# Performance work log

Hardware: AMD Instinct MI355X
Metric: run time of the kernel (lower is better)

The kernel has to match this reference:

```python
import jax, jax.numpy as jnp
import numpy as np

N = 150000   # total supergraph nodes (entities+events+chains)
D = 128      # embed_size
H = 4        # attention heads
DH = D // H  # head dim
E = 300000   # edges per layer
L = 4        # layer_specs length
A = 8        # edge attr dim
T = 10       # num_edge_type
TIME_SCALE = 24.0
SLOPE = 0.2  # negative_slope


def setup_inputs() -> dict:
    key = jax.random.key(0)
    ks = jax.random.split(key, 16)
    nrm = lambda k, s, sc=1.0: jax.random.normal(k, s, dtype=jnp.float32) * sc
    return {
        'x': nrm(ks[0], (N, D), 0.1),
        'Wq': nrm(ks[1], (L, D, D), D ** -0.5),
        'Wk': nrm(ks[2], (L, D, D), D ** -0.5),
        'Wv': nrm(ks[3], (L, D, D), D ** -0.5),
        'Wskip': nrm(ks[4], (L, D, D), D ** -0.5),
        'Wa': nrm(ks[5], (L, A, D), 0.1),
        'time_w': nrm(ks[6], (D,)),
        'time_b': nrm(ks[7], (D,), 0.1),
        'dist_w': nrm(ks[8], (D,)),
        'dist_b': nrm(ks[9], (D,), 0.1),
        'type_table': nrm(ks[10], (T, D), 0.1),
        'bn_gamma': jnp.ones((L, D), jnp.float32),
        'bn_beta': jnp.zeros((L, D), jnp.float32),
        'beta': jnp.full((L,), 0.5, jnp.float32),
        'edge_attr': jax.random.uniform(ks[11], (L, E, A), dtype=jnp.float32),
        'edge_dt': jax.random.uniform(ks[12], (L, E), dtype=jnp.float32) * TIME_SCALE,
        'edge_ds': jax.random.uniform(ks[13], (L, E), dtype=jnp.float32) * 10.0,
        'edge_index': jax.random.randint(ks[14], (L, 2, E), 0, N),
        'edge_type': jax.random.randint(ks[15], (L, E), 0, T),
    }


def _layer(x, Wq, Wk, Wv, Wskip, Wa, time_w, time_b, dist_w, dist_b,
           type_table, gamma, bvec, beta, attr, dt, ds, ei, et):
    n = x.shape[0]
    src, dst = ei[0], ei[1]
    # continuous time / distance encoders: cos basis (TimeEncoder / 'time' DistanceEncoder)
    te = jnp.cos((dt / TIME_SCALE)[:, None] * time_w + time_b)   # [E,D]
    de = jnp.cos(ds[:, None] * dist_w + dist_b)                  # [E,D]
    # 'add' edge/time fusion: attr MLP + time + dist + edge-type embeddings
    edge_feat = attr @ Wa + te + de + type_table[et]             # [E,D]
    kv_in = x[src] + edge_feat                                   # gather + fuse
    q = (x @ Wq).reshape(n, H, DH)[dst]                          # [E,H,DH]
    k = (kv_in @ Wk).reshape(-1, H, DH)
    v = (kv_in @ Wv).reshape(-1, H, DH)
    logits = (q * k).sum(-1) * (DH ** -0.5)                      # [E,H]
    logits = jnp.where(logits >= 0, logits, SLOPE * logits)      # leaky_relu(negative_slope)
    # segment softmax over incoming edges of each destination node
    m = jax.ops.segment_max(logits, dst, num_segments=n)
    a = jnp.exp(logits - m[dst])
    denom = jax.ops.segment_sum(a, dst, num_segments=n)
    a = a / denom[dst]
    agg = jax.ops.segment_sum(a[..., None] * v, dst, num_segments=n).reshape(n, D)
    # beta-weighted residual (learn_beta) with skip projection
    out = beta * (x @ Wskip) + (1.0 - beta) * agg
    # BatchNorm1d (training-mode batch stats) + ReLU
    mu = out.mean(0)
    var = out.var(0)
    out = (out - mu) * jax.lax.rsqrt(var + 1e-5) * gamma + bvec
    return jax.nn.relu(out)


def reference(x, Wq, Wk, Wv, Wskip, Wa, time_w, time_b, dist_w, dist_b,
              type_table, bn_gamma, bn_beta, beta, edge_attr, edge_dt,
              edge_ds, edge_index, edge_type):
    for l in range(L):  # entity2event, event2event, event2chain (time filter), chain2chain
        x = _layer(x, Wq[l], Wk[l], Wv[l], Wskip[l], Wa[l],
                   time_w, time_b, dist_w, dist_b, type_table,
                   bn_gamma[l], bn_beta[l], beta[l],
                   edge_attr[l], edge_dt[l], edge_ds[l],
                   edge_index[l], edge_type[l])
    return x
```

## Files before the change

kernel.cpp:

```cpp
#include <hip/hip_runtime.h>

typedef unsigned int u32;
typedef unsigned short u16;
typedef short bf16x8 __attribute__((ext_vector_type(8)));
typedef float f32x4 __attribute__((ext_vector_type(4)));

#define N_NODES 150000
#define E_EDGES 300000
#define L_CNT   151552
#define ETILES  9375
#define NTILES  4688

__device__ __forceinline__ float blo(u32 u){ return __uint_as_float(u << 16); }
__device__ __forceinline__ float bhi(u32 u){ return __uint_as_float(u & 0xffff0000u); }
__device__ __forceinline__ float b2f(u16 h){ return __uint_as_float(((u32)h) << 16); }
__device__ __forceinline__ u16 f2bf(float f){
  u32 u = __float_as_uint(f);
  return (u16)((u + 0x7fffu + ((u >> 16) & 1u)) >> 16);
}
__device__ __forceinline__ u32 pack2(float a, float b){
  return (u32)f2bf(a) | ((u32)f2bf(b) << 16);
}

__device__ __forceinline__ f32x4 mfma16(bf16x8 a, bf16x8 b, f32x4 c){
  return __builtin_amdgcn_mfma_f32_16x16x32_bf16(a, b, c, 0, 0, 0);
}

__device__ __forceinline__ int opsw(int r, int k){ return (r * 128 + k) ^ ((r & 7) << 3); }
__device__ __forceinline__ int csw(int r, int n){ return (r * 128 + n) ^ (((r >> 2) & 3) << 3); }

__global__ __launch_bounds__(256)
void k_wt(const float* __restrict__ Wq, const float* __restrict__ Wk,
          const float* __restrict__ Wv, const float* __restrict__ Ws,
          u16* __restrict__ Wt)
{
  const int m = blockIdx.x;
  const float* src = (m < 4 ? Wq : m < 8 ? Wk : m < 12 ? Wv : Ws)
                     + (size_t)(m & 3) * 16384;
  u16* dst = Wt + (size_t)m * 16384;
  const int t = threadIdx.x;
  for (int i = 0; i < 16; ++i) {
    int idx = i * 256 + t;
    int n = idx >> 5;
    int k4 = (idx & 31) << 2;
    ushort4 o;
    o.x = f2bf(src[(k4 + 0) * 128 + n]);
    o.y = f2bf(src[(k4 + 1) * 128 + n]);
    o.z = f2bf(src[(k4 + 2) * 128 + n]);
    o.w = f2bf(src[(k4 + 3) * 128 + n]);
    *(ushort4*)(dst + n * 128 + k4) = o;
  }
}


__global__ __launch_bounds__(256)
void k_hist(const int* __restrict__ eidx, int* __restrict__ counts)
{
  const int l = blockIdx.y;
  const int e = blockIdx.x * 256 + threadIdx.x;
  if (e < E_EDGES) {
    int dst = eidx[(size_t)l * 2 * E_EDGES + E_EDGES + e];
    atomicAdd(&counts[(size_t)l * L_CNT + dst], 1);
  }
}

__global__ __launch_bounds__(256)
void k_scan1(const int* __restrict__ counts, int* __restrict__ rowptr,
             int* __restrict__ bsum)
{
  __shared__ int sh[256];
  const int b = blockIdx.x, l = blockIdx.y;
  const int t = threadIdx.x;
  const int* c = counts + (size_t)l * L_CNT + b * 2048;
  int* rp = rowptr + (size_t)l * L_CNT + b * 2048;
  int v[8]; int s = 0;
  #pragma unroll
  for (int j = 0; j < 8; ++j) { v[j] = c[t * 8 + j]; s += v[j]; }
  sh[t] = s; __syncthreads();
  for (int off = 1; off < 256; off <<= 1) {
    int x = (t >= off) ? sh[t - off] : 0;
    __syncthreads();
    sh[t] += x;
    __syncthreads();
  }
  int excl = (t == 0) ? 0 : sh[t - 1];
  if (t == 255) bsum[l * 128 + b] = sh[255];
  int run = excl;
  #pragma unroll
  for (int j = 0; j < 8; ++j) { rp[t * 8 + j] = run; run += v[j]; }
}

__global__ __launch_bounds__(128)
void k_scan2(int* __restrict__ bsum)
{
  __shared__ int sh[128];
  const int l = blockIdx.x, t = threadIdx.x;
  int v = (t < 74) ? bsum[l * 128 + t] : 0;
  sh[t] = v; __syncthreads();
  for (int off = 1; off < 128; off <<= 1) {
    int x = (t >= off) ? sh[t - off] : 0;
    __syncthreads();
    sh[t] += x;
    __syncthreads();
  }
  int excl = (t == 0) ? 0 : sh[t - 1];
  if (t < 74) bsum[l * 128 + t] = excl;
}

__global__ __launch_bounds__(256)
void k_scan3(int* __restrict__ rowptr, int* __restrict__ tmp,
             const int* __restrict__ bsum)
{
  const int l = blockIdx.y;
  const int q = blockIdx.x * 256 + threadIdx.x;
  int v = rowptr[(size_t)l * L_CNT + q] + bsum[l * 128 + (q >> 11)];
  rowptr[(size_t)l * L_CNT + q] = v;
  tmp[(size_t)l * L_CNT + q] = v;
}

__global__ __launch_bounds__(256)
void k_scatter(const int* __restrict__ srcP, const int* __restrict__ dstP,
               const int* __restrict__ etP, const float* __restrict__ dtP,
               const float* __restrict__ dsP, const float* __restrict__ attrP,
               int* __restrict__ tmpL, u32* __restrict__ meta)
{
  const int e = blockIdx.x * 256 + threadIdx.x;
  if (e < E_EDGES) {
    int dst = dstP[e];
    int pos = atomicAdd(&tmpL[dst], 1);
    int src = srcP[e];
    int et  = etP[e];
    float dtn = dtP[e] * (1.0f / 24.0f);
    float dsv = dsP[e];
    float4 aA = *(const float4*)(attrP + (size_t)e * 8);
    float4 aB = *(const float4*)(attrP + (size_t)e * 8 + 4);
    uint4 r0, r1;
    r0.x = (u32)src;
    r0.y = (u32)dst | ((u32)et << 20);
    r0.z = __float_as_uint(dtn);
    r0.w = __float_as_uint(dsv);
    r1.x = pack2(aA.x, aA.y); r1.y = pack2(aA.z, aA.w);
    r1.z = pack2(aB.x, aB.y); r1.w = pack2(aB.z, aB.w);
    u32* mp = meta + (size_t)pos * 8;
    *(uint4*)mp = r0;
    *(uint4*)(mp + 4) = r1;
  }
}

template<int XF32>
__global__ __launch_bounds__(256)
void k_kvin(const void* __restrict__ xg, const float* __restrict__ Wa,
            const float* __restrict__ tw, const float* __restrict__ tb,
            const float* __restrict__ dw, const float* __restrict__ db,
            const float* __restrict__ ttab, const u32* __restrict__ meta,
            u16* __restrict__ kvV)
{
  const int idx = blockIdx.x * 256 + threadIdx.x;
  const int e = idx >> 4;
  const int c8 = (idx & 15) << 3;
  const u32* mp = meta + (size_t)e * 8;
  uint4 m0 = *(const uint4*)mp;
  uint4 m1 = *(const uint4*)(mp + 4);
  const int src = (int)m0.x;
  const int et = (int)(m0.y >> 20);
  const float dtn = __uint_as_float(m0.z);
  const float dss = __uint_as_float(m0.w);
  float aa[8] = { blo(m1.x), bhi(m1.x), blo(m1.y), bhi(m1.y),
                  blo(m1.z), bhi(m1.z), blo(m1.w), bhi(m1.w) };
  const float4 twA = *(const float4*)(tw + c8);
  const float4 twB = *(const float4*)(tw + c8 + 4);
  const float4 tbA = *(const float4*)(tb + c8);
  const float4 tbB = *(const float4*)(tb + c8 + 4);
  const float4 dwA = *(const float4*)(dw + c8);
  const float4 dwB = *(const float4*)(dw + c8 + 4);
  const float4 dbA = *(const float4*)(db + c8);
  const float4 dbB = *(const float4*)(db + c8 + 4);
  const float4 ttA = *(const float4*)(ttab + et * 128 + c8);
  const float4 ttB = *(const float4*)(ttab + et * 128 + c8 + 4);
  float f[8];
  f[0] = __cosf(fmaf(dtn, twA.x, tbA.x)) + __cosf(fmaf(dss, dwA.x, dbA.x)) + ttA.x;
  f[1] = __cosf(fmaf(dtn, twA.y, tbA.y)) + __cosf(fmaf(dss, dwA.y, dbA.y)) + ttA.y;
  f[2] = __cosf(fmaf(dtn, twA.z, tbA.z)) + __cosf(fmaf(dss, dwA.z, dbA.z)) + ttA.z;
  f[3] = __cosf(fmaf(dtn, twA.w, tbA.w)) + __cosf(fmaf(dss, dwA.w, dbA.w)) + ttA.w;
  f[4] = __cosf(fmaf(dtn, twB.x, tbB.x)) + __cosf(fmaf(dss, dwB.x, dbB.x)) + ttB.x;
  f[5] = __cosf(fmaf(dtn, twB.y, tbB.y)) + __cosf(fmaf(dss, dwB.y, dbB.y)) + ttB.y;
  f[6] = __cosf(fmaf(dtn, twB.z, tbB.z)) + __cosf(fmaf(dss, dwB.z, dbB.z)) + ttB.z;
  f[7] = __cosf(fmaf(dtn, twB.w, tbB.w)) + __cosf(fmaf(dss, dwB.w, dbB.w)) + ttB.w;
  #pragma unroll
  for (int a = 0; a < 8; ++a) {
    float4 wA = *(const float4*)(Wa + a * 128 + c8);
    float4 wB = *(const float4*)(Wa + a * 128 + c8 + 4);
    f[0] = fmaf(aa[a], wA.x, f[0]);
    f[1] = fmaf(aa[a], wA.y, f[1]);
    f[2] = fmaf(aa[a], wA.z, f[2]);
    f[3] = fmaf(aa[a], wA.w, f[3]);
    f[4] = fmaf(aa[a], wB.x, f[4]);
    f[5] = fmaf(aa[a], wB.y, f[5]);
    f[6] = fmaf(aa[a], wB.z, f[6]);
    f[7] = fmaf(aa[a], wB.w, f[7]);
  }
  float xv[8];
  if (XF32) {
    float4 xA = *(const float4*)((const float*)xg + (size_t)src * 128 + c8);
    float4 xB = *(const float4*)((const float*)xg + (size_t)src * 128 + c8 + 4);
    xv[0] = xA.x; xv[1] = xA.y; xv[2] = xA.z; xv[3] = xA.w;
    xv[4] = xB.x; xv[5] = xB.y; xv[6] = xB.z; xv[7] = xB.w;
  } else {
    uint4 xr = *(const uint4*)((const u16*)xg + (size_t)src * 128 + c8);
    xv[0] = blo(xr.x); xv[1] = bhi(xr.x); xv[2] = blo(xr.y); xv[3] = bhi(xr.y);
    xv[4] = blo(xr.z); xv[5] = bhi(xr.z); xv[6] = blo(xr.w); xv[7] = bhi(xr.w);
  }
  uint4 o;
  o.x = pack2(xv[0] + f[0], xv[1] + f[1]);
  o.y = pack2(xv[2] + f[2], xv[3] + f[3]);
  o.z = pack2(xv[4] + f[4], xv[5] + f[5]);
  o.w = pack2(xv[6] + f[6], xv[7] + f[7]);
  *(uint4*)(kvV + (size_t)e * 128 + c8) = o;
}


template<int XF32>
__global__ __launch_bounds__(128, 2)
void gemm_qs(const void* __restrict__ xg, const u16* __restrict__ WtQ,
             const u16* __restrict__ WtS, u16* __restrict__ Qo,
             u16* __restrict__ So)
{
  __shared__ __align__(16) u16 As[4160];
  __shared__ __align__(16) u16 Bs[4160];
  const int t = threadIdx.x;
  const int w = t >> 6, lane = t & 63;
  const int lr = lane & 15, hi = lane >> 4;
  const int row0 = blockIdx.x * 32;
  const int nr = min(32, N_NODES - row0);
  const u16* Wt = w ? WtS : WtQ;
  u16* C = w ? So : Qo;

  bf16x8 wt[8][4];
  #pragma unroll
  for (int nb = 0; nb < 8; ++nb)
    #pragma unroll
    for (int ks = 0; ks < 4; ++ks)
      wt[nb][ks] = *(const bf16x8*)(Wt + (nb * 16 + lr) * 128 + ks * 32 + hi * 8);

  #pragma unroll
  for (int i = 0; i < 4; ++i) {
    int idx = i * 128 + t;
    int r = idx >> 4, c8 = (idx & 15) << 3;
    if (r < nr) {
      if (XF32) {
        float4 vA = *(const float4*)((const float*)xg + (size_t)(row0 + r) * 128 + c8);
        float4 vB = *(const float4*)((const float*)xg + (size_t)(row0 + r) * 128 + c8 + 4);
        uint4 o;
        o.x = pack2(vA.x, vA.y); o.y = pack2(vA.z, vA.w);
        o.z = pack2(vB.x, vB.y); o.w = pack2(vB.z, vB.w);
        *(uint4*)(As + opsw(r, c8)) = o;
      } else {
        uint4 v = *(const uint4*)((const u16*)xg + (size_t)(row0 + r) * 128 + c8);
        *(uint4*)(As + opsw(r, c8)) = v;
      }
    } else {
      *(uint4*)(As + opsw(r, c8)) = make_uint4(0, 0, 0, 0);
    }
  }
  __syncthreads();

  f32x4 acc[2][8];
  #pragma unroll
  for (int a = 0; a < 2; ++a)
    #pragma unroll
    for (int b = 0; b < 8; ++b) {
      acc[a][b][0] = 0.f; acc[a][b][1] = 0.f;
      acc[a][b][2] = 0.f; acc[a][b][3] = 0.f;
    }
  #pragma unroll
  for (int ks = 0; ks < 4; ++ks) {
    const int kb = ks * 32 + hi * 8;
    bf16x8 a0 = *(const bf16x8*)(As + opsw(lr, kb));
    bf16x8 a1 = *(const bf16x8*)(As + opsw(16 + lr, kb));
    #pragma unroll
    for (int nb = 0; nb < 8; ++nb) {
      acc[0][nb] = mfma16(a0, wt[nb][ks], acc[0][nb]);
      acc[1][nb] = mfma16(a1, wt[nb][ks], acc[1][nb]);
    }
  }
  __syncthreads();

  u16* Cs = w ? Bs : As;
  const int g4 = hi << 2;
  #pragma unroll
  for (int mt = 0; mt < 2; ++mt)
    #pragma unroll
    for (int nt = 0; nt < 8; ++nt)
      #pragma unroll
      for (int j = 0; j < 4; ++j)
        Cs[csw(mt * 16 + g4 + j, nt * 16 + lr)] = f2bf(acc[mt][nt][j]);
  #pragma unroll
  for (int i = 0; i < 8; ++i) {
    int idx = i * 64 + lane;
    int r = idx >> 4, n8 = (idx & 15) << 3;
    if (r < nr) {
      uint4 v = *(const uint4*)(Cs + csw(r, n8));
      *(uint4*)(C + (size_t)(row0 + r) * 128 + n8) = v;
    }
  }
}


__global__ __launch_bounds__(128, 2)
void edge_kv(const u16* __restrict__ WtK, const u16* __restrict__ WtV,
             const u32* __restrict__ meta, const u16* __restrict__ Qb,
             u16* __restrict__ kvV, float* __restrict__ logits)
{
  __shared__ __align__(16) u16 KVs[4160];
  __shared__ __align__(16) u16 Qs[4160];
  __shared__ __align__(16) u16 Cs[4160];
  __shared__ int dstSh[32];
  const int t = threadIdx.x;
  const int w = t >> 6, lane = t & 63;
  const int lr = lane & 15, hi = lane >> 4;
  const int e0 = blockIdx.x * 32;
  const u16* Wt = w ? WtV : WtK;

  bf16x8 wt[8][4];
  #pragma unroll
  for (int nb = 0; nb < 8; ++nb)
    #pragma unroll
    for (int ks = 0; ks < 4; ++ks)
      wt[nb][ks] = *(const bf16x8*)(Wt + (nb * 16 + lr) * 128 + ks * 32 + hi * 8);

  if (t < 32)
    dstSh[t] = (int)(meta[(size_t)(e0 + t) * 8 + 1] & 0xFFFFFu);

  #pragma unroll
  for (int i = 0; i < 4; ++i) {
    int idx = i * 128 + t;
    int r = idx >> 4, c8 = (idx & 15) << 3;
    uint4 v = *(const uint4*)(kvV + (size_t)(e0 + r) * 128 + c8);
    *(uint4*)(KVs + opsw(r, c8)) = v;
  }
  if (w == 0) {
    #pragma unroll
    for (int i = 0; i < 8; ++i) {
      int idx = i * 64 + lane;
      int r = idx >> 4, c8 = (idx & 15) << 3;
      int qrow = dstSh[r];
      uint4 qv = *(const uint4*)(Qb + (size_t)qrow * 128 + c8);
      *(uint4*)(Qs + opsw(r, c8)) = qv;
    }
  }
  __syncthreads();

  if (w == 0) {
    #pragma unroll
    for (int eb = 0; eb < 2; ++eb) {
      f32x4 kacc[8];
      #pragma unroll
      for (int b = 0; b < 8; ++b) {
        kacc[b][0] = 0.f; kacc[b][1] = 0.f; kacc[b][2] = 0.f; kacc[b][3] = 0.f;
      }
      #pragma unroll
      for (int ks = 0; ks < 4; ++ks) {
        bf16x8 ef = *(const bf16x8*)(KVs + opsw(eb * 16 + lr, ks * 32 + hi * 8));
        #pragma unroll
        for (int nb = 0; nb < 8; ++nb)
          kacc[nb] = mfma16(wt[nb][ks], ef, kacc[nb]);
      }
      const int el = eb * 16 + lr;
      float hs[4] = {0.f, 0.f, 0.f, 0.f};
      #pragma unroll
      for (int nb = 0; nb < 8; ++nb) {
        ushort4 q = *(const ushort4*)(Qs + opsw(el, nb * 16 + hi * 4));
        hs[nb >> 1] += b2f(q.x) * kacc[nb][0] + b2f(q.y) * kacc[nb][1]
                     + b2f(q.z) * kacc[nb][2] + b2f(q.w) * kacc[nb][3];
      }
      #pragma unroll
      for (int h = 0; h < 4; ++h) {
        hs[h] += __shfl_xor(hs[h], 16, 64);
        hs[h] += __shfl_xor(hs[h], 32, 64);
        hs[h] *= 0.17677669529663687f;
        hs[h] = (hs[h] >= 0.f) ? hs[h] : 0.2f * hs[h];
      }
      if (lane < 16)
        *(float4*)(logits + (size_t)(e0 + el) * 4) = make_float4(hs[0], hs[1], hs[2], hs[3]);
    }
  } else {
    const int g4 = hi << 2;
    #pragma unroll
    for (int mt = 0; mt < 2; ++mt) {
      f32x4 vacc[8];
      #pragma unroll
      for (int b = 0; b < 8; ++b) {
        vacc[b][0] = 0.f; vacc[b][1] = 0.f; vacc[b][2] = 0.f; vacc[b][3] = 0.f;
      }
      #pragma unroll
      for (int ks = 0; ks < 4; ++ks) {
        bf16x8 af = *(const bf16x8*)(KVs + opsw(mt * 16 + lr, ks * 32 + hi * 8));
        #pragma unroll
        for (int nb = 0; nb < 8; ++nb)
          vacc[nb] = mfma16(af, wt[nb][ks], vacc[nb]);
      }
      #pragma unroll
      for (int nt = 0; nt < 8; ++nt)
        #pragma unroll
        for (int j = 0; j < 4; ++j)
          Cs[csw(mt * 16 + g4 + j, nt * 16 + lr)] = f2bf(vacc[nt][j]);
    }
    #pragma unroll
    for (int i = 0; i < 8; ++i) {
      int idx = i * 64 + lane;
      int r = idx >> 4, n8 = (idx & 15) << 3;
      uint4 v = *(const uint4*)(Cs + csw(r, n8));
      *(uint4*)(kvV + (size_t)(e0 + r) * 128 + n8) = v;
    }
  }
}

__global__ __launch_bounds__(256)
void node_agg(const u16* __restrict__ Vs, const float* __restrict__ logits,
              const int* __restrict__ rowptr, const u16* __restrict__ S,
              const float* __restrict__ betaP, float* __restrict__ pre,
              float* __restrict__ colsum, float* __restrict__ colsumsq)
{
  __shared__ float red[1024];
  const int t = threadIdx.x;
  const int g = t >> 5;
  const int lane = t & 31;
  const int d0 = lane * 4;
  const int h = lane >> 3;
  const float beta = *betaP;
  const float omb = 1.f - beta;
  float s4[4] = {0.f, 0.f, 0.f, 0.f};
  float q4[4] = {0.f, 0.f, 0.f, 0.f};
  for (int rep = 0; rep < 16; ++rep) {
    int n = blockIdx.x * 128 + rep * 8 + g;
    if (n < N_NODES) {
      int rs = rowptr[n], re = rowptr[n + 1];
      float m = -1e30f;
      for (int i = rs; i < re; ++i)
        m = fmaxf(m, logits[(size_t)i * 4 + h]);
      float den = 0.f;
      float a0 = 0.f, a1 = 0.f, a2 = 0.f, a3 = 0.f;
      for (int i = rs; i < re; ++i) {
        float wgt = __expf(logits[(size_t)i * 4 + h] - m);
        den += wgt;
        ushort4 v = *(const ushort4*)(Vs + (size_t)i * 128 + d0);
        a0 = fmaf(wgt, b2f(v.x), a0);
        a1 = fmaf(wgt, b2f(v.y), a1);
        a2 = fmaf(wgt, b2f(v.z), a2);
        a3 = fmaf(wgt, b2f(v.w), a3);
      }
      float inv = (den > 0.f) ? (omb / den) : 0.f;
      ushort4 sv = *(const ushort4*)(S + (size_t)n * 128 + d0);
      float p0 = fmaf(beta, b2f(sv.x), a0 * inv);
      float p1 = fmaf(beta, b2f(sv.y), a1 * inv);
      float p2 = fmaf(beta, b2f(sv.z), a2 * inv);
      float p3 = fmaf(beta, b2f(sv.w), a3 * inv);
      *(float4*)(pre + (size_t)n * 128 + d0) = make_float4(p0, p1, p2, p3);
      s4[0] += p0; s4[1] += p1; s4[2] += p2; s4[3] += p3;
      q4[0] += p0 * p0; q4[1] += p1 * p1; q4[2] += p2 * p2; q4[3] += p3 * p3;
    }
  }
  *(float4*)(&red[g * 128 + d0]) = make_float4(s4[0], s4[1], s4[2], s4[3]);
  __syncthreads();
  if (t < 128) {
    float tot = 0.f;
    #pragma unroll
    for (int gg = 0; gg < 8; ++gg) tot += red[gg * 128 + t];
    atomicAdd(&colsum[t], tot);
  }
  __syncthreads();
  *(float4*)(&red[g * 128 + d0]) = make_float4(q4[0], q4[1], q4[2], q4[3]);
  __syncthreads();
  if (t < 128) {
    float tot = 0.f;
    #pragma unroll
    for (int gg = 0; gg < 8; ++gg) tot += red[gg * 128 + t];
    atomicAdd(&colsumsq[t], tot);
  }
}

template<int LAST>
__global__ __launch_bounds__(256)
void bn_apply(const float* __restrict__ pre, const float* __restrict__ colsum,
              const float* __restrict__ colsumsq, const float* __restrict__ gamma,
              const float* __restrict__ bvec, u16* __restrict__ outbf,
              float* __restrict__ outf)
{
  const int idx = blockIdx.x * 256 + threadIdx.x;
  const int n = idx >> 5;
  const int d0 = (idx & 31) * 4;
  const float invN = 1.f / 150000.f;
  float4 p = *(const float4*)(pre + (size_t)n * 128 + d0);
  float4 cs = *(const float4*)(colsum + d0);
  float4 cq = *(const float4*)(colsumsq + d0);
  float4 gm = *(const float4*)(gamma + d0);
  float4 bv = *(const float4*)(bvec + d0);
  float mu, var, y;
  mu = cs.x * invN; var = cq.x * invN - mu * mu;
  y = (p.x - mu) * rsqrtf(var + 1e-5f) * gm.x + bv.x; p.x = fmaxf(y, 0.f);
  mu = cs.y * invN; var = cq.y * invN - mu * mu;
  y = (p.y - mu) * rsqrtf(var + 1e-5f) * gm.y + bv.y; p.y = fmaxf(y, 0.f);
  mu = cs.z * invN; var = cq.z * invN - mu * mu;
  y = (p.z - mu) * rsqrtf(var + 1e-5f) * gm.z + bv.z; p.z = fmaxf(y, 0.f);
  mu = cs.w * invN; var = cq.w * invN - mu * mu;
  y = (p.w - mu) * rsqrtf(var + 1e-5f) * gm.w + bv.w; p.w = fmaxf(y, 0.f);
  if (LAST) {
    *(float4*)(outf + (size_t)n * 128 + d0) = p;
  } else {
    ushort4 o;
    o.x = f2bf(p.x); o.y = f2bf(p.y); o.z = f2bf(p.z); o.w = f2bf(p.w);
    *(ushort4*)(outbf + (size_t)n * 128 + d0) = o;
  }
}

extern "C" void kernel_launch(void* const* d_in, const int* in_sizes, int n_in,
                              void* d_out, int out_size, void* d_ws, size_t ws_size,
                              hipStream_t stream)
{
  const float* x0    = (const float*)d_in[0];
  const float* Wq    = (const float*)d_in[1];
  const float* Wk    = (const float*)d_in[2];
  const float* Wv    = (const float*)d_in[3];
  const float* Wsk   = (const float*)d_in[4];
  const float* Wa    = (const float*)d_in[5];
  const float* tw    = (const float*)d_in[6];
  const float* tb    = (const float*)d_in[7];
  const float* dw    = (const float*)d_in[8];
  const float* db    = (const float*)d_in[9];
  const float* ttab  = (const float*)d_in[10];
  const float* gam   = (const float*)d_in[11];
  const float* bet   = (const float*)d_in[12];
  const float* betaP = (const float*)d_in[13];
  const float* attr  = (const float*)d_in[14];
  const float* dt    = (const float*)d_in[15];
  const float* dsv   = (const float*)d_in[16];
  const int*   eidx  = (const int*)d_in[17];
  const int*   etyp  = (const int*)d_in[18];

  char* p = (char*)d_ws;
  u16* xbf  = (u16*)p;       p += 38400000;
  u16* Q    = (u16*)p;       p += 38400000;
  u16* S    = (u16*)p;       p += 38400000;
  u16* kvV  = (u16*)p;       p += 76800000;
  float* logits = (float*)p; p += 4800000;
  int* rowptr = (int*)p;     p += 4 * L_CNT * 4;
  int* tmp    = (int*)p;     p += 4 * L_CNT * 4;
  int* bsum   = (int*)p;     p += 4 * 128 * 4;
  float* colsum   = (float*)p; p += 512;
  float* colsumsq = (float*)p; p += 512;
  u16* Wt = (u16*)p;         p += 16 * 16384 * 2;
  u32* meta = (u32*)p;       p += (size_t)E_EDGES * 32;

  float* pre = (float*)d_out;

  k_wt<<<16, 256, 0, stream>>>(Wq, Wk, Wv, Wsk, Wt);
  hipMemsetAsync(tmp, 0, 4 * L_CNT * 4, stream);
  k_hist<<<dim3(1172, 4), 256, 0, stream>>>(eidx, tmp);
  k_scan1<<<dim3(74, 4), 256, 0, stream>>>(tmp, rowptr, bsum);
  k_scan2<<<4, 128, 0, stream>>>(bsum);
  k_scan3<<<dim3(592, 4), 256, 0, stream>>>(rowptr, tmp, bsum);

  for (int l = 0; l < 4; ++l) {
    const int* srcA = eidx + (size_t)l * 600000;
    const int* dstA = srcA + 300000;
    const int* rpl = rowptr + (size_t)l * L_CNT;
    const u16* WtQl = Wt + (size_t)l * 16384;
    const u16* WtKl = Wt + (size_t)(4 + l) * 16384;
    const u16* WtVl = Wt + (size_t)(8 + l) * 16384;
    const u16* WtSl = Wt + (size_t)(12 + l) * 16384;
    const float* Wal = Wa + (size_t)l * 1024;

    k_scatter<<<1172, 256, 0, stream>>>(
        srcA, dstA, etyp + (size_t)l * 300000, dt + (size_t)l * 300000,
        dsv + (size_t)l * 300000, attr + (size_t)l * 2400000,
        tmp + (size_t)l * L_CNT, meta);

    hipMemsetAsync(colsum, 0, 1024, stream);

    if (l == 0) {
      k_kvin<1><<<18750, 256, 0, stream>>>((const void*)x0, Wal, tw, tb, dw, db,
                                           ttab, meta, kvV);
      gemm_qs<1><<<NTILES, 128, 0, stream>>>((const void*)x0, WtQl, WtSl, Q, S);
    } else {
      k_kvin<0><<<18750, 256, 0, stream>>>((const void*)xbf, Wal, tw, tb, dw, db,
                                           ttab, meta, kvV);
      gemm_qs<0><<<NTILES, 128, 0, stream>>>((const void*)xbf, WtQl, WtSl, Q, S);
    }

    edge_kv<<<ETILES, 128, 0, stream>>>(WtKl, WtVl, meta, Q, kvV, logits);

    node_agg<<<1172, 256, 0, stream>>>(kvV, logits, rpl, S, betaP + l,
                                       pre, colsum, colsumsq);

    if (l < 3)
      bn_apply<0><<<18750, 256, 0, stream>>>(pre, colsum, colsumsq,
                                             gam + (size_t)l * 128,
                                             bet + (size_t)l * 128, xbf, nullptr);
    else
      bn_apply<1><<<18750, 256, 0, stream>>>(pre, colsum, colsumsq,
                                             gam + (size_t)l * 128,
                                             bet + (size_t)l * 128,
                                             nullptr, (float*)d_out);
  }
}
```

Measured before the change: 1.495 ms.

## Make gemm_qs and edge_kv persistent with register prefetch of next tile

Converts the Q/skip GEMM and edge K/V kernels into persistent grid-stride loops over 2048 blocks, so the register-held weight fragments are loaded once per block instead of once per 32-row tile. The next tile's inputs (and dst indices) are prefetched into registers while the current tile computes. In edge_kv the Q-gather moves to the V wave and the V output staging reuses the Qs buffer, which drops one shared array. The cost is extra barriers and register pressure from the prefetch buffers, which may reduce occupancy.

```diff
diff --git a/kernel.cpp b/kernel.cpp
--- a/kernel.cpp
+++ b/kernel.cpp
@@ -230,8 +230,6 @@
   const int t = threadIdx.x;
   const int w = t >> 6, lane = t & 63;
   const int lr = lane & 15, hi = lane >> 4;
-  const int row0 = blockIdx.x * 32;
-  const int nr = min(32, N_NODES - row0);
   const u16* Wt = w ? WtS : WtQ;
   u16* C = w ? So : Qo;
 
@@ -242,66 +240,83 @@
     for (int ks = 0; ks < 4; ++ks)
       wt[nb][ks] = *(const bf16x8*)(Wt + (nb * 16 + lr) * 128 + ks * 32 + hi * 8);
 
-  #pragma unroll
-  for (int i = 0; i < 4; ++i) {
-    int idx = i * 128 + t;
-    int r = idx >> 4, c8 = (idx & 15) << 3;
-    if (r < nr) {
+  const int r_ = (t >> 4) & 7;
+
+  uint4 xp[4];
+  auto PREF = [&](int tile){
+    int row0 = tile * 32;
+    #pragma unroll
+    for (int i = 0; i < 4; ++i) {
+      int idx = i * 128 + t;
+      int r = idx >> 4, c8 = (idx & 15) << 3;
+      int rr = row0 + r; if (rr >= N_NODES) rr = N_NODES - 1;
       if (XF32) {
-        float4 vA = *(const float4*)((const float*)xg + (size_t)(row0 + r) * 128 + c8);
-        float4 vB = *(const float4*)((const float*)xg + (size_t)(row0 + r) * 128 + c8 + 4);
-        uint4 o;
-        o.x = pack2(vA.x, vA.y); o.y = pack2(vA.z, vA.w);
-        o.z = pack2(vB.x, vB.y); o.w = pack2(vB.z, vB.w);
-        *(uint4*)(As + opsw(r, c8)) = o;
+        float4 vA = *(const float4*)((const float*)xg + (size_t)rr * 128 + c8);
+        float4 vB = *(const float4*)((const float*)xg + (size_t)rr * 128 + c8 + 4);
+        xp[i].x = pack2(vA.x, vA.y); xp[i].y = pack2(vA.z, vA.w);
+        xp[i].z = pack2(vB.x, vB.y); xp[i].w = pack2(vB.z, vB.w);
       } else {
-        uint4 v = *(const uint4*)((const u16*)xg + (size_t)(row0 + r) * 128 + c8);
-        *(uint4*)(As + opsw(r, c8)) = v;
-      }
-    } else {
-      *(uint4*)(As + opsw(r, c8)) = make_uint4(0, 0, 0, 0);
-    }
-  }
-  __syncthreads();
-
-  f32x4 acc[2][8];
-  #pragma unroll
-  for (int a = 0; a < 2; ++a)
-    #pragma unroll
-    for (int b = 0; b < 8; ++b) {
-      acc[a][b][0] = 0.f; acc[a][b][1] = 0.f;
-      acc[a][b][2] = 0.f; acc[a][b][3] = 0.f;
-    }
-  #pragma unroll
-  for (int ks = 0; ks < 4; ++ks) {
-    const int kb = ks * 32 + hi * 8;
-    bf16x8 a0 = *(const bf16x8*)(As + opsw(lr, kb));
-    bf16x8 a1 = *(const bf16x8*)(As + opsw(16 + lr, kb));
-    #pragma unroll
-    for (int nb = 0; nb < 8; ++nb) {
-      acc[0][nb] = mfma16(a0, wt[nb][ks], acc[0][nb]);
-      acc[1][nb] = mfma16(a1, wt[nb][ks], acc[1][nb]);
-    }
-  }
-  __syncthreads();
-
-  u16* Cs = w ? Bs : As;
-  const int g4 = hi << 2;
-  #pragma unroll
-  for (int mt = 0; mt < 2; ++mt)
-    #pragma unroll
-    for (int nt = 0; nt < 8; ++nt)
-      #pragma unroll
-      for (int j = 0; j < 4; ++j)
-        Cs[csw(mt * 16 + g4 + j, nt * 16 + lr)] = f2bf(acc[mt][nt][j]);
-  #pragma unroll
-  for (int i = 0; i < 8; ++i) {
-    int idx = i * 64 + lane;
-    int r = idx >> 4, n8 = (idx & 15) << 3;
-    if (r < nr) {
-      uint4 v = *(const uint4*)(Cs + csw(r, n8));
-      *(uint4*)(C + (size_t)(row0 + r) * 128 + n8) = v;
-    }
+        xp[i] = *(const uint4*)((const u16*)xg + (size_t)rr * 128 + c8);
+      }
+    }
+  };
+
+  int tile = blockIdx.x;
+  if (tile >= NTILES) return;
+  PREF(tile);
+  for (; tile < NTILES; tile += gridDim.x) {
+    const int row0 = tile * 32;
+    const int nr = min(32, N_NODES - row0);
+    #pragma unroll
+    for (int i = 0; i < 4; ++i) {
+      int idx = i * 128 + t;
+      int r = idx >> 4, c8 = (idx & 15) << 3;
+      *(uint4*)(As + opsw(r, c8)) = (r < nr) ? xp[i] : make_uint4(0, 0, 0, 0);
+    }
+    int ntile = tile + gridDim.x;
+    if (ntile < NTILES) PREF(ntile);
+    __syncthreads();
+
+    f32x4 acc[2][8];
+    #pragma unroll
+    for (int a = 0; a < 2; ++a)
+      #pragma unroll
+      for (int b = 0; b < 8; ++b) {
+        acc[a][b][0] = 0.f; acc[a][b][1] = 0.f;
+        acc[a][b][2] = 0.f; acc[a][b][3] = 0.f;
+      }
+    #pragma unroll
+    for (int ks = 0; ks < 4; ++ks) {
+      const int kb = ks * 32 + hi * 8;
+      bf16x8 a0 = *(const bf16x8*)(As + opsw(lr, kb));
+      bf16x8 a1 = *(const bf16x8*)(As + opsw(16 + lr, kb));
+      #pragma unroll
+      for (int nb = 0; nb < 8; ++nb) {
+        acc[0][nb] = mfma16(a0, wt[nb][ks], acc[0][nb]);
+        acc[1][nb] = mfma16(a1, wt[nb][ks], acc[1][nb]);
+      }
+    }
+    __syncthreads();
+
+    u16* Cs = w ? Bs : As;
+    const int g4 = hi << 2;
+    #pragma unroll
+    for (int mt = 0; mt < 2; ++mt)
+      #pragma unroll
+      for (int nt = 0; nt < 8; ++nt)
+        #pragma unroll
+        for (int j = 0; j < 4; ++j)
+          Cs[csw(mt * 16 + g4 + j, nt * 16 + lr)] = f2bf(acc[mt][nt][j]);
+    #pragma unroll
+    for (int i = 0; i < 8; ++i) {
+      int idx = i * 64 + lane;
+      int r = idx >> 4, n8 = (idx & 15) << 3;
+      if (r < nr) {
+        uint4 v = *(const uint4*)(Cs + csw(r, n8));
+        *(uint4*)(C + (size_t)(row0 + r) * 128 + n8) = v;
+      }
+    }
+    __syncthreads();
   }
 }
 
@@ -313,12 +328,10 @@
 {
   __shared__ __align__(16) u16 KVs[4160];
   __shared__ __align__(16) u16 Qs[4160];
-  __shared__ __align__(16) u16 Cs[4160];
   __shared__ int dstSh[32];
   const int t = threadIdx.x;
   const int w = t >> 6, lane = t & 63;
   const int lr = lane & 15, hi = lane >> 4;
-  const int e0 = blockIdx.x * 32;
   const u16* Wt = w ? WtV : WtK;
 
   bf16x8 wt[8][4];
@@ -328,90 +341,118 @@
     for (int ks = 0; ks < 4; ++ks)
       wt[nb][ks] = *(const bf16x8*)(Wt + (nb * 16 + lr) * 128 + ks * 32 + hi * 8);
 
-  if (t < 32)
-    dstSh[t] = (int)(meta[(size_t)(e0 + t) * 8 + 1] & 0xFFFFFu);
-
-  #pragma unroll
-  for (int i = 0; i < 4; ++i) {
-    int idx = i * 128 + t;
-    int r = idx >> 4, c8 = (idx & 15) << 3;
-    uint4 v = *(const uint4*)(kvV + (size_t)(e0 + r) * 128 + c8);
-    *(uint4*)(KVs + opsw(r, c8)) = v;
-  }
-  if (w == 0) {
-    #pragma unroll
-    for (int i = 0; i < 8; ++i) {
-      int idx = i * 64 + lane;
+  uint4 kvp[4];
+  int dstReg = 0;
+  auto PREF = [&](int tile){
+    int e0 = tile * 32;
+    #pragma unroll
+    for (int i = 0; i < 4; ++i) {
+      int idx = i * 128 + t;
       int r = idx >> 4, c8 = (idx & 15) << 3;
-      int qrow = dstSh[r];
-      uint4 qv = *(const uint4*)(Qb + (size_t)qrow * 128 + c8);
-      *(uint4*)(Qs + opsw(r, c8)) = qv;
-    }
-  }
-  __syncthreads();
-
-  if (w == 0) {
-    #pragma unroll
-    for (int eb = 0; eb < 2; ++eb) {
-      f32x4 kacc[8];
-      #pragma unroll
-      for (int b = 0; b < 8; ++b) {
-        kacc[b][0] = 0.f; kacc[b][1] = 0.f; kacc[b][2] = 0.f; kacc[b][3] = 0.f;
-      }
+      kvp[i] = *(const uint4*)(kvV + (size_t)(e0 + r) * 128 + c8);
+    }
+    if (w == 1 && lane < 32)
+      dstReg = (int)(meta[(size_t)(e0 + lane) * 8 + 1] & 0xFFFFFu);
+  };
+
+  int tile = blockIdx.x;
+  if (tile >= ETILES) return;
+  PREF(tile);
+  for (; tile < ETILES; tile += gridDim.x) {
+    const int e0 = tile * 32;
+    #pragma unroll
+    for (int i = 0; i < 4; ++i) {
+      int idx = i * 128 + t;
+      int r = idx >> 4, c8 = (idx & 15) << 3;
+      *(uint4*)(KVs + opsw(r, c8)) = kvp[i];
+    }
+    if (w == 1 && lane < 32) dstSh[lane] = dstReg;
+    int ntile = tile + gridDim.x;
+    if (ntile < ETILES) PREF(ntile);
+    if (w == 1) {
+      #pragma unroll
+      for (int i = 0; i < 8; ++i) {
+        int idx = i * 64 + lane;
+        int r = idx >> 4, c8 = (idx & 15) << 3;
+        int qrow = dstSh[r];
+        uint4 qv = *(const uint4*)(Qb + (size_t)qrow * 128 + c8);
+        *(uint4*)(Qs + opsw(r, c8)) = qv;
+      }
+    }
+    __syncthreads();
+
+    if (w == 0) {
+      #pragma unroll
+      for (int eb = 0; eb < 2; ++eb) {
+        f32x4 kacc[8];
+        #pragma unroll
+        for (int b = 0; b < 8; ++b) {
+          kacc[b][0] = 0.f; kacc[b][1] = 0.f; kacc[b][2] = 0.f; kacc[b][3] = 0.f;
+        }
+        #pragma unroll
+        for (int ks = 0; ks < 4; ++ks) {
+          bf16x8 ef = *(const bf16x8*)(KVs + opsw(eb * 16 + lr, ks * 32 + hi * 8));
+          #pragma unroll
+          for (int nb = 0; nb < 8; ++nb)
+            kacc[nb] = mfma16(wt[nb][ks], ef, kacc[nb]);
+        }
+        const int el = eb * 16 + lr;
+        float hs[4] = {0.f, 0.f, 0.f, 0.f};
+        #pragma unroll
+        for (int nb = 0; nb < 8; ++nb) {
+          ushort4 q = *(const ushort4*)(Qs + opsw(el, nb * 16 + hi * 4));
+          hs[nb >> 1] += b2f(q.x) * kacc[nb][0] + b2f(q.y) * kacc[nb][1]
+                       + b2f(q.z) * kacc[nb][2] + b2f(q.w) * kacc[nb][3];
+        }
+        #pragma unroll
+        for (int h = 0; h < 4; ++h) {
+          hs[h] += __shfl_xor(hs[h], 16, 64);
+          hs[h] += __shfl_xor(hs[h], 32, 64);
+          hs[h] *= 0.17677669529663687f;
+          hs[h] = (hs[h] >= 0.f) ? hs[h] : 0.2f * hs[h];
+        }
+        if (lane < 16)
+          *(float4*)(logits + (size_t)(e0 + el) * 4) = make_float4(hs[0], hs[1], hs[2], hs[3]);
+      }
+      __syncthreads();
+    } else {
+      f32x4 vacc[2][8];
+      #pragma unroll
+      for (int a = 0; a < 2; ++a)
+        #pragma unroll
+        for (int b = 0; b < 8; ++b) {
+          vacc[a][b][0] = 0.f; vacc[a][b][1] = 0.f;
+          vacc[a][b][2] = 0.f; vacc[a][b][3] = 0.f;
+        }
       #pragma unroll
       for (int ks = 0; ks < 4; ++ks) {
-        bf16x8 ef = *(const bf16x8*)(KVs + opsw(eb * 16 + lr, ks * 32 + hi * 8));
-        #pragma unroll
-        for (int nb = 0; nb < 8; ++nb)
-          kacc[nb] = mfma16(wt[nb][ks], ef, kacc[nb]);
-      }
-      const int el = eb * 16 + lr;
-      float hs[4] = {0.f, 0.f, 0.f, 0.f};
-      #pragma unroll
-      for (int nb = 0; nb < 8; ++nb) {
-        ushort4 q = *(const ushort4*)(Qs + opsw(el, nb * 16 + hi * 4));
-        hs[nb >> 1] += b2f(q.x) * kacc[nb][0] + b2f(q.y) * kacc[nb][1]
-                     + b2f(q.z) * kacc[nb][2] + b2f(q.w) * kacc[nb][3];
-      }
-      #pragma unroll
-      for (int h = 0; h < 4; ++h) {
-        hs[h] += __shfl_xor(hs[h], 16, 64);
-        hs[h] += __shfl_xor(hs[h], 32, 64);
-        hs[h] *= 0.17677669529663687f;
-        hs[h] = (hs[h] >= 0.f) ? hs[h] : 0.2f * hs[h];
-      }
-      if (lane < 16)
-        *(float4*)(logits + (size_t)(e0 + el) * 4) = make_float4(hs[0], hs[1], hs[2], hs[3]);
-    }
-  } else {
-    const int g4 = hi << 2;
-    #pragma unroll
-    for (int mt = 0; mt < 2; ++mt) {
-      f32x4 vacc[8];
-      #pragma unroll
-      for (int b = 0; b < 8; ++b) {
-        vacc[b][0] = 0.f; vacc[b][1] = 0.f; vacc[b][2] = 0.f; vacc[b][3] = 0.f;
-      }
-      #pragma unroll
-      for (int ks = 0; ks < 4; ++ks) {
-        bf16x8 af = *(const bf16x8*)(KVs + opsw(mt * 16 + lr, ks * 32 + hi * 8));
-        #pragma unroll
-        for (int nb = 0; nb < 8; ++nb)
-          vacc[nb] = mfma16(af, wt[nb][ks], vacc[nb]);
-      }
-      #pragma unroll
-      for (int nt = 0; nt < 8; ++nt)
-        #pragma unroll
-        for (int j = 0; j < 4; ++j)
-          Cs[csw(mt * 16 + g4 + j, nt * 16 + lr)] = f2bf(vacc[nt][j]);
-    }
-    #pragma unroll
-    for (int i = 0; i < 8; ++i) {
-      int idx = i * 64 + lane;
-      int r = idx >> 4, n8 = (idx & 15) << 3;
-      uint4 v = *(const uint4*)(Cs + csw(r, n8));
-      *(uint4*)(kvV + (size_t)(e0 + r) * 128 + n8) = v;
-    }
+        const int kb = ks * 32 + hi * 8;
+        bf16x8 a0 = *(const bf16x8*)(KVs + opsw(lr, kb));
+        bf16x8 a1 = *(const bf16x8*)(KVs + opsw(16 + lr, kb));
+        #pragma unroll
+        for (int nb = 0; nb < 8; ++nb) {
+          vacc[0][nb] = mfma16(a0, wt[nb][ks], vacc[0][nb]);
+          vacc[1][nb] = mfma16(a1, wt[nb][ks], vacc[1][nb]);
+        }
+      }
+      __syncthreads();
+      const int g4 = hi << 2;
+      #pragma unroll
+      for (int mt = 0; mt < 2; ++mt)
+        #pragma unroll
+        for (int nt = 0; nt < 8; ++nt)
+          #pragma unroll
+          for (int j = 0; j < 4; ++j)
+            Qs[csw(mt * 16 + g4 + j, nt * 16 + lr)] = f2bf(vacc[mt][nt][j]);
+      #pragma unroll
+      for (int i = 0; i < 8; ++i) {
+        int idx = i * 64 + lane;
+        int r = idx >> 4, n8 = (idx & 15) << 3;
+        uint4 v = *(const uint4*)(Qs + csw(r, n8));
+        *(uint4*)(kvV + (size_t)(e0 + r) * 128 + n8) = v;
+      }
+    }
+    __syncthreads();
   }
 }
 
@@ -580,14 +621,14 @@
     if (l == 0) {
       k_kvin<1><<<18750, 256, 0, stream>>>((const void*)x0, Wal, tw, tb, dw, db,
                                            ttab, meta, kvV);
-      gemm_qs<1><<<NTILES, 128, 0, stream>>>((const void*)x0, WtQl, WtSl, Q, S);
+      gemm_qs<1><<<2048, 128, 0, stream>>>((const void*)x0, WtQl, WtSl, Q, S);
     } else {
       k_kvin<0><<<18750, 256, 0, stream>>>((const void*)xbf, Wal, tw, tb, dw, db,
                                            ttab, meta, kvV);
-      gemm_qs<0><<<NTILES, 128, 0, stream>>>((const void*)xbf, WtQl, WtSl, Q, S);
-    }
-
-    edge_kv<<<ETILES, 128, 0, stream>>>(WtKl, WtVl, meta, Q, kvV, logits);
+      gemm_qs<0><<<2048, 128, 0, stream>>>((const void*)xbf, WtQl, WtSl, Q, S);
+    }
+
+    edge_kv<<<2048, 128, 0, stream>>>(WtKl, WtVl, meta, Q, kvV, logits);
 
     node_agg<<<1172, 256, 0, stream>>>(kvV, logits, rpl, S, betaP + l,
                                        pre, colsum, colsumsq);
```

Result: slower. 2.339 ms (+56.5%).
